# Performance work log

Hardware: AMD Instinct MI355X
Metric: run time of the kernel (lower is better)

Reference implementation:

```python
import jax, jax.numpy as jnp
import numpy as np

NUM_BINS = 128  # 32 mid-band bins + 96 bottom-band bins
LN_EPS = 1e-5


def _mlp_scores(desc, W1, b1, g1, be1, W2, b2, Ws, bs):
    # Linear -> LayerNorm -> SiLU -> Linear -> score head
    h = desc @ W1 + b1
    mu = h.mean(-1, keepdims=True)
    var = h.var(-1, keepdims=True)
    h = (h - mu) * jax.lax.rsqrt(var + LN_EPS) * g1 + be1
    h = h * jax.nn.sigmoid(h)  # SiLU
    feat = h @ W2 + b2
    scores = (feat @ Ws + bs)[..., 0]  # [B, N]
    return scores


def _grid_ids(kpts, H, W):
    x = kpts[..., 0]
    y = kpts[..., 1]
    mid = (y > 0.2 * H) & (y <= 0.5 * H)
    btm = y > 0.5 * H
    mgx = jnp.clip((x / W * 8).astype(jnp.int32), 0, 7)
    mgy = jnp.clip(((y - 0.2 * H) / (0.3 * H) * 4).astype(jnp.int32), 0, 3)
    bgx = jnp.clip((x / W * 16).astype(jnp.int32), 0, 15)
    bgy = jnp.clip(((y - 0.5 * H) / (0.5 * H) * 6).astype(jnp.int32), 0, 5)
    gid = jnp.where(btm, 32 + bgy * 16 + bgx, jnp.where(mid, mgy * 8 + mgx, -1))
    return gid  # [B, N], -1 = not in any grid band


def _select_one(scores, gid, top_k):
    # strict-'>' loop in the original), then compact + top-k fallback.
    N = scores.shape[0]
    valid = gid >= 0
    seg = jnp.where(valid, gid, NUM_BINS)  # dump invalid pts in dummy bin
    binmax = jax.ops.segment_max(scores, seg, num_segments=NUM_BINS + 1)
    is_win = valid & (scores == binmax[seg])
    winner_idx = jax.ops.segment_min(
        jnp.where(is_win, jnp.arange(N), N), seg, num_segments=NUM_BINS + 1
    )[:NUM_BINS]  # N = empty bin sentinel
    bin_valid = winner_idx < N
    # stable sort: non-empty bins first, preserving bin order
    order = jnp.argsort((~bin_valid).astype(jnp.int32))
    winners = winner_idx[order]  # [NUM_BINS], trailing sentinels
    num_sel = jnp.sum(bin_valid)
    # mask out already-selected winners, top-k fallback on the rest
    win_mask = jnp.zeros(N, bool).at[jnp.where(bin_valid, winner_idx, N)].set(True, mode='drop')
    rem = jnp.where(win_mask, -1e10, scores)
    _, extra = jax.lax.top_k(rem, top_k)
    j = jnp.arange(top_k)
    sel = jnp.where(
        j < num_sel,
        winners[jnp.clip(j, 0, NUM_BINS - 1)],
        extra[jnp.clip(j - num_sel, 0, top_k - 1)],
    )
    return sel  # [top_k]


def setup_inputs() -> dict:
    key = jax.random.key(0)
    ks = jax.random.split(key, 4)
    B, N, IN, OUT = 8, 50000, 256, 128
    H, W = 376, 1241
    kpts = jax.random.uniform(ks[0], (B, N, 2), jnp.float32) * jnp.array([W, H], jnp.float32)
    desc = jax.random.normal(ks[1], (B, N, IN), jnp.float32)
    kw = jax.random.split(ks[2], 3)
    W1 = 0.01 * jax.random.normal(kw[0], (IN, 256), jnp.float32)
    b1 = jnp.zeros((256,), jnp.float32)
    g1 = jnp.ones((256,), jnp.float32)
    be1 = jnp.zeros((256,), jnp.float32)
    W2 = 0.01 * jax.random.normal(kw[1], (256, OUT), jnp.float32)
    b2 = jnp.zeros((OUT,), jnp.float32)
    Ws = 0.001 * jax.random.normal(kw[2], (OUT, 1), jnp.float32)
    bs = jnp.zeros((1,), jnp.float32)
    return {"kpts": kpts, "desc": desc, "H": H, "W": W, "top_k": 128,
            "W1": W1, "b1": b1, "g1": g1, "be1": be1,
            "W2": W2, "b2": b2, "Ws": Ws, "bs": bs}


def reference(kpts, desc, H, W, top_k, W1, b1, g1, be1, W2, b2, Ws, bs):
    scores = _mlp_scores(desc, W1, b1, g1, be1, W2, b2, Ws, bs)  # [B,N]
    gid = _grid_ids(kpts, H, W)  # [B,N]
    indices = jax.vmap(lambda s, g: _select_one(s, g, top_k))(scores, gid)  # [B,top_k]
    final_feat = jnp.take_along_axis(desc, indices[:, :, None], axis=1)  # [B,top_k,256]
    final_kpts = jnp.take_along_axis(kpts, indices[:, :, None], axis=1)  # [B,top_k,2]
    return final_feat, final_kpts, indices
```

## Files before the change

kernel.cpp:

```cpp
#include <hip/hip_runtime.h>

#define THREADS 256

typedef short bf16x8 __attribute__((ext_vector_type(8)));
typedef float f32x4 __attribute__((ext_vector_type(4)));

__device__ __forceinline__ unsigned short f2bf(float x) {
    unsigned u = __float_as_uint(x);
    return (unsigned short)((u + 0x7FFFu + ((u >> 16) & 1u)) >> 16);
}
__device__ __forceinline__ float bf2f(unsigned short h) {
    return __uint_as_float(((unsigned)h) << 16);
}
__device__ __forceinline__ unsigned score_key(float s) {
    unsigned u = __float_as_uint(s);
    return (u & 0x80000000u) ? ~u : (u | 0x80000000u);
}

__device__ __forceinline__ void split8(const float* __restrict__ f, bf16x8& hv, bf16x8& lv) {
    union { unsigned w[4]; bf16x8 v; } H, L;
#pragma unroll
    for (int q = 0; q < 4; ++q) {
        const float x0 = f[2 * q], x1 = f[2 * q + 1];
        const unsigned b0 = __float_as_uint(x0), b1_ = __float_as_uint(x1);
        const unsigned u0 = b0 + 0x7FFFu + ((b0 >> 16) & 1u);
        const unsigned u1 = b1_ + 0x7FFFu + ((b1_ >> 16) & 1u);
        const float h0 = __uint_as_float(u0 & 0xFFFF0000u);
        const float h1 = __uint_as_float(u1 & 0xFFFF0000u);
        const unsigned l0 = f2bf(x0 - h0), l1 = f2bf(x1 - h1);
        H.w[q] = (u0 >> 16) | ((u1 >> 16) << 16);
        L.w[q] = l0 | (l1 << 16);
    }
    hv = H.v; lv = L.v;
}

__device__ __forceinline__ void async_cp16(const uint4* g, uint4* l) {
    __builtin_amdgcn_global_load_lds(
        (const __attribute__((address_space(1))) unsigned int*)g,
        (__attribute__((address_space(3))) unsigned int*)l, 16, 0, 0);
}

__global__ void prep_kernel(const float* __restrict__ W2, const float* __restrict__ b2,
                            const float* __restrict__ Ws, const float* __restrict__ bs,
                            float* __restrict__ v, int OUT) {
    int j = threadIdx.x;
    float acc = 0.f;
    for (int o = 0; o < OUT; ++o) acc += W2[j * OUT + o] * Ws[o];
    v[j] = acc;
    if (j == 0) {
        float c = bs[0];
        for (int o = 0; o < OUT; ++o) c += b2[o] * Ws[o];
        v[256] = c;
    }
}

__global__ void prep_w1frag(const float* __restrict__ W1, uint4* __restrict__ wfrag) {
    const int s = blockIdx.x * 256 + threadIdx.x;
    const int rem = s & 2047;
    const int kt = s >> 11;
    const int c = rem >> 6;
    const int lane = rem & 63;
    const int h = c >> 4;
    const int nt = c & 15;
    const int col = nt * 16 + (lane & 15);
    const int kb = kt * 32 + (lane >> 4) * 8;
    unsigned pk[4];
#pragma unroll
    for (int q = 0; q < 4; ++q) {
        float x0 = W1[(size_t)(kb + 2 * q) * 256 + col];
        float x1 = W1[(size_t)(kb + 2 * q + 1) * 256 + col];
        unsigned short a0, a1;
        if (h == 0) { a0 = f2bf(x0); a1 = f2bf(x1); }
        else {
            a0 = f2bf(x0 - bf2f(f2bf(x0)));
            a1 = f2bf(x1 - bf2f(f2bf(x1)));
        }
        pk[q] = (unsigned)a0 | ((unsigned)a1 << 16);
    }
    wfrag[s] = make_uint4(pk[0], pk[1], pk[2], pk[3]);
}

__global__ void init_bins(unsigned long long* __restrict__ bins, int n) {
    int i = blockIdx.x * blockDim.x + threadIdx.x;
    if (i < n) bins[i] = 0ULL;
}

__global__ __launch_bounds__(256, 2) void score_kernel(
    const float* __restrict__ desc, const float* __restrict__ kpts,
    const uint4* __restrict__ wfrag,
    const float* __restrict__ b1, const float* __restrict__ g1, const float* __restrict__ be1,
    const int* __restrict__ Hp, const int* __restrict__ Wp,
    const float* __restrict__ v,
    float* __restrict__ scores, unsigned long long* __restrict__ bins,
    int N, int total)
{
    __shared__ uint4 BS[2][32 * 64];
    __shared__ float b1L[256], g1L[256], beL[256], vL[256];

    const int t = threadIdx.x;
    const int lane = t & 63;
    const int w = t >> 6;
    const int l15 = lane & 15, q4 = lane >> 4;
    const int wrow0 = blockIdx.x * 128 + w * 32;

    b1L[t] = b1[t]; g1L[t] = g1[t]; beL[t] = be1[t]; vL[t] = v[t];

    {
        const uint4* bsrc = wfrag + (w * 8) * 64 + lane;
#pragma unroll
        for (int j = 0; j < 8; ++j)
            async_cp16(bsrc + j * 64, &BS[0][(w * 8 + j) * 64]);
    }

    const int rA0 = min(wrow0 + l15, total - 1);
    const int rA1 = min(wrow0 + 16 + l15, total - 1);
    const float* pa0 = desc + (size_t)rA0 * 256 + q4 * 8;
    const float* pa1 = desc + (size_t)rA1 * 256 + q4 * 8;
    float4 a00 = *(const float4*)pa0, a01 = *(const float4*)(pa0 + 4);
    float4 a10 = *(const float4*)pa1, a11 = *(const float4*)(pa1 + 4);

    __syncthreads();

    f32x4 acc[2][16];
#pragma unroll
    for (int n = 0; n < 16; ++n) {
        const float bc = b1L[n * 16 + l15];
        acc[0][n] = (f32x4){bc, bc, bc, bc};
        acc[1][n] = (f32x4){bc, bc, bc, bc};
    }

    for (int kt = 0; kt < 8; ++kt) {
        const int cur = kt & 1;
        if (kt < 7) {
            const uint4* bsrc = wfrag + (size_t)(kt + 1) * 2048 + (w * 8) * 64 + lane;
#pragma unroll
            for (int j = 0; j < 8; ++j)
                async_cp16(bsrc + j * 64, &BS[cur ^ 1][(w * 8 + j) * 64]);
        }
        bf16x8 ah[2], al[2];
        {
            float f0[8] = {a00.x, a00.y, a00.z, a00.w, a01.x, a01.y, a01.z, a01.w};
            split8(f0, ah[0], al[0]);
            float f1[8] = {a10.x, a10.y, a10.z, a10.w, a11.x, a11.y, a11.z, a11.w};
            split8(f1, ah[1], al[1]);
        }
        if (kt < 7) {
            const float* q0 = pa0 + (kt + 1) * 32;
            const float* q1 = pa1 + (kt + 1) * 32;
            a00 = *(const float4*)q0; a01 = *(const float4*)(q0 + 4);
            a10 = *(const float4*)q1; a11 = *(const float4*)(q1 + 4);
        }
#pragma unroll
        for (int g = 0; g < 4; ++g) {
            bf16x8 bh[4], bl[4];
#pragma unroll
            for (int j = 0; j < 4; ++j) {
                bh[j] = *(const bf16x8*)&BS[cur][(g * 4 + j) * 64 + lane];
                bl[j] = *(const bf16x8*)&BS[cur][(16 + g * 4 + j) * 64 + lane];
            }
#pragma unroll
            for (int p = 0; p < 4; ++p) {
#pragma unroll
                for (int j = 0; j < 4; ++j)
#pragma unroll
                    for (int m = 0; m < 2; ++m) {
                        const bf16x8 aa = (p & 2) ? al[m] : ah[m];
                        const bf16x8 bb = (p & 1) ? bl[j] : bh[j];
                        acc[m][g * 4 + j] =
                            __builtin_amdgcn_mfma_f32_16x16x32_bf16(aa, bb, acc[m][g * 4 + j], 0, 0, 0);
                    }
            }
        }
        __syncthreads();
    }

    const float Wf = (float)Wp[0];
    const int Hi = Hp[0];
    const float t02 = (float)(0.2 * (double)Hi);
    const float t05 = (float)(0.5 * (double)Hi);
    const float t03 = (float)(0.3 * (double)Hi);
    const float cterm = v[256];

#pragma unroll
    for (int m = 0; m < 2; ++m)
#pragma unroll
        for (int r = 0; r < 4; ++r) {
            float sx = 0.f, sq = 0.f;
#pragma unroll
            for (int n = 0; n < 16; ++n) {
                const float x = acc[m][n][r];
                sx += x; sq = fmaf(x, x, sq);
            }
#pragma unroll
            for (int mask = 1; mask <= 8; mask <<= 1) {
                sx += __shfl_xor(sx, mask);
                sq += __shfl_xor(sq, mask);
            }
            const float mu = sx * (1.f / 256.f);
            const float var = sq * (1.f / 256.f) - mu * mu;
            const float rs = 1.f / sqrtf(var + 1e-5f);
            float dot = 0.f;
#pragma unroll
            for (int n = 0; n < 16; ++n) {
                const int c = n * 16 + l15;
                const float hv = (acc[m][n][r] - mu) * rs * g1L[c] + beL[c];
                const float sg = 1.f / (1.f + __expf(-hv));
                dot = fmaf(vL[c], hv * sg, dot);
            }
#pragma unroll
            for (int mask = 1; mask <= 8; mask <<= 1) dot += __shfl_xor(dot, mask);

            if (l15 == 0) {
                const int row = wrow0 + m * 16 + q4 * 4 + r;
                if (row < total) {
                    const float sc = dot + cterm;
                    scores[row] = sc;
                    const float x = kpts[(size_t)row * 2 + 0];
                    const float y = kpts[(size_t)row * 2 + 1];
                    int g = -1;
                    if (y > t05) {
                        int bgx = (int)(x / Wf * 16.f); bgx = min(max(bgx, 0), 15);
                        int bgy = (int)((y - t05) / t05 * 6.f); bgy = min(max(bgy, 0), 5);
                        g = 32 + bgy * 16 + bgx;
                    } else if (y > t02) {
                        int mgx = (int)(x / Wf * 8.f); mgx = min(max(mgx, 0), 7);
                        int mgy = (int)((y - t02) / t03 * 4.f); mgy = min(max(mgy, 0), 3);
                        g = mgy * 8 + mgx;
                    }
                    if (g >= 0) {
                        const int bb = row / N;
                        const int n = row - bb * N;
                        const unsigned long long pk =
                            ((unsigned long long)score_key(sc) << 32) | (unsigned)(~(unsigned)n);
                        atomicMax(&bins[bb * 128 + g], pk);
                    }
                }
            }
        }
}

__global__ __launch_bounds__(256) void finalize_kernel(
    const float* __restrict__ scores, const unsigned long long* __restrict__ bins,
    const float* __restrict__ desc, const float* __restrict__ kpts,
    const int* __restrict__ tkp, float* __restrict__ out, int B, int N)
{
    const int b = blockIdx.x, t = threadIdx.x;
    const int topk = tkp[0];
    __shared__ int selL[512];
    __shared__ int nselS;
    __shared__ unsigned long long red[256];
    __shared__ unsigned long long binL[128];

    if (t < 128) binL[t] = bins[b * 128 + t];
    __syncthreads();
    if (t == 0) {
        int c = 0;
        for (int i = 0; i < 128; ++i)
            if ((binL[i] >> 32) != 0ULL) selL[c++] = (int)(~(unsigned)binL[i]);
        nselS = c;
    }
    __syncthreads();
    const int nsel = nselS;

    for (int need = nsel; need < topk; ++need) {
        unsigned long long best = 0ULL;
        for (int i = t; i < N; i += THREADS) {
            bool taken = false;
            for (int s2 = 0; s2 < need; ++s2)
                if (selL[s2] == i) { taken = true; break; }
            if (!taken) {
                const unsigned long long pk =
                    ((unsigned long long)score_key(scores[(size_t)b * N + i]) << 32)
                    | (unsigned)(~(unsigned)i);
                if (pk > best) best = pk;
            }
        }
        red[t] = best;
        __syncthreads();
        for (int off = 128; off > 0; off >>= 1) {
            if (t < off) { if (red[t + off] > red[t]) red[t] = red[t + off]; }
            __syncthreads();
        }
        if (t == 0) selL[need] = (int)(~(unsigned)red[0]);
        __syncthreads();
    }

    float* o_feat = out;
    float* o_kpts = out + (size_t)B * topk * 256;
    float* o_idx  = out + (size_t)B * topk * 258;
    for (int e = t; e < topk * 64; e += THREADS) {
        const int j = e >> 6, q4 = e & 63;
        const int n = selL[j];
        *(float4*)&o_feat[((size_t)b * topk + j) * 256 + q4 * 4] =
            *(const float4*)&desc[((size_t)b * N + n) * 256 + q4 * 4];
    }
    for (int j = t; j < topk; j += THREADS) {
        const int n = selL[j];
        o_kpts[((size_t)b * topk + j) * 2 + 0] = kpts[((size_t)b * N + n) * 2 + 0];
        o_kpts[((size_t)b * topk + j) * 2 + 1] = kpts[((size_t)b * N + n) * 2 + 1];
        o_idx[(size_t)b * topk + j] = (float)n;
    }
}

extern "C" void kernel_launch(void* const* d_in, const int* in_sizes, int n_in,
                              void* d_out, int out_size, void* d_ws, size_t ws_size,
                              hipStream_t stream) {
    const float* kpts = (const float*)d_in[0];
    const float* desc = (const float*)d_in[1];
    const int*   Hp   = (const int*)d_in[2];
    const int*   Wp   = (const int*)d_in[3];
    const int*   tkp  = (const int*)d_in[4];
    const float* W1   = (const float*)d_in[5];
    const float* b1   = (const float*)d_in[6];
    const float* g1   = (const float*)d_in[7];
    const float* be1  = (const float*)d_in[8];
    const float* W2   = (const float*)d_in[9];
    const float* b2   = (const float*)d_in[10];
    const float* Ws   = (const float*)d_in[11];
    const float* bs   = (const float*)d_in[12];

    const int total = in_sizes[1] / 256;
    const int BT    = out_size / 259;
    const int B     = BT / 128;
    const int N     = total / B;
    const int OUT   = in_sizes[11];

    float* ws_v      = (float*)d_ws;
    float* ws_scores = ws_v + 512;
    size_t off = ((size_t)(512 + total) * 4 + 255) & ~(size_t)255;
    unsigned long long* ws_bins = (unsigned long long*)((char*)d_ws + off);
    size_t off2 = (off + (size_t)B * 128 * 8 + 255) & ~(size_t)255;
    uint4* ws_wfrag = (uint4*)((char*)d_ws + off2);

    prep_kernel<<<1, 256, 0, stream>>>(W2, b2, Ws, bs, ws_v, OUT);
    prep_w1frag<<<64, 256, 0, stream>>>(W1, ws_wfrag);
    init_bins<<<(B * 128 + 255) / 256, 256, 0, stream>>>(ws_bins, B * 128);
    score_kernel<<<(total + 127) / 128, 256, 0, stream>>>(
        desc, kpts, ws_wfrag, b1, g1, be1, Hp, Wp, ws_v, ws_scores, ws_bins, N, total);
    finalize_kernel<<<B, 256, 0, stream>>>(ws_scores, ws_bins, desc, kpts, tkp,
                                           (float*)d_out, B, N);
}
```

Before: 430.4 us.

## Switch score GEMM to 32x32x16 MFMA with re-laid-out W1 fragments

Each wave's 32-row tile now uses 32x32x16 bf16 MFMA instructions instead of two 16-row tiles of 16x16x32. The W1 fragment layout in the prep kernel is rebuilt to match, and the LayerNorm/SiLU epilogue is rewritten for the 32x32 accumulator layout with wider shuffle reductions. It also uses the library bf16 conversion for the hi/lo split and raises wave priority around the MFMA bursts. The aim is to cut LDS reads of B fragments and per-instruction overhead in the split-precision GEMM, at the cost of more accumulator registers per lane and a more complex row mapping.

```diff
diff --git a/kernel.cpp b/kernel.cpp
--- a/kernel.cpp
+++ b/kernel.cpp
@@ -1,9 +1,10 @@
 #include <hip/hip_runtime.h>
+#include <hip/hip_bf16.h>
 
 #define THREADS 256
 
 typedef short bf16x8 __attribute__((ext_vector_type(8)));
-typedef float f32x4 __attribute__((ext_vector_type(4)));
+typedef float f32x16 __attribute__((ext_vector_type(16)));
 
 __device__ __forceinline__ unsigned short f2bf(float x) {
     unsigned u = __float_as_uint(x);
@@ -17,19 +18,18 @@
     return (u & 0x80000000u) ? ~u : (u | 0x80000000u);
 }
 
-__device__ __forceinline__ void split8(const float* __restrict__ f, bf16x8& hv, bf16x8& lv) {
-    union { unsigned w[4]; bf16x8 v; } H, L;
-#pragma unroll
-    for (int q = 0; q < 4; ++q) {
-        const float x0 = f[2 * q], x1 = f[2 * q + 1];
-        const unsigned b0 = __float_as_uint(x0), b1_ = __float_as_uint(x1);
-        const unsigned u0 = b0 + 0x7FFFu + ((b0 >> 16) & 1u);
-        const unsigned u1 = b1_ + 0x7FFFu + ((b1_ >> 16) & 1u);
-        const float h0 = __uint_as_float(u0 & 0xFFFF0000u);
-        const float h1 = __uint_as_float(u1 & 0xFFFF0000u);
-        const unsigned l0 = f2bf(x0 - h0), l1 = f2bf(x1 - h1);
-        H.w[q] = (u0 >> 16) | ((u1 >> 16) << 16);
-        L.w[q] = l0 | (l1 << 16);
+__device__ __forceinline__ void split8n(const float4& fa, const float4& fb,
+                                        bf16x8& hv, bf16x8& lv) {
+    const float f[8] = {fa.x, fa.y, fa.z, fa.w, fb.x, fb.y, fb.z, fb.w};
+    union { unsigned short u[8]; bf16x8 v; } H, L;
+#pragma unroll
+    for (int j = 0; j < 8; ++j) {
+        __hip_bfloat16 hb = __float2bfloat16(f[j]);
+        const unsigned short hr = reinterpret_cast<const unsigned short&>(hb);
+        const float hf = __uint_as_float(((unsigned)hr) << 16);
+        __hip_bfloat16 lb = __float2bfloat16(f[j] - hf);
+        H.u[j] = hr;
+        L.u[j] = reinterpret_cast<const unsigned short&>(lb);
     }
     hv = H.v; lv = L.v;
 }
@@ -56,21 +56,21 @@
 
 __global__ void prep_w1frag(const float* __restrict__ W1, uint4* __restrict__ wfrag) {
     const int s = blockIdx.x * 256 + threadIdx.x;
-    const int rem = s & 2047;
     const int kt = s >> 11;
-    const int c = rem >> 6;
-    const int lane = rem & 63;
-    const int h = c >> 4;
-    const int nt = c & 15;
-    const int col = nt * 16 + (lane & 15);
-    const int kb = kt * 32 + (lane >> 4) * 8;
+    const int c = (s >> 6) & 31;
+    const int lane = s & 63;
+    const int hl = c >> 4;
+    const int nt = (c >> 1) & 7;
+    const int kc = c & 1;
+    const int col = nt * 32 + (lane & 31);
+    const int k0 = kt * 32 + kc * 16 + (lane >> 5) * 8;
     unsigned pk[4];
 #pragma unroll
     for (int q = 0; q < 4; ++q) {
-        float x0 = W1[(size_t)(kb + 2 * q) * 256 + col];
-        float x1 = W1[(size_t)(kb + 2 * q + 1) * 256 + col];
+        float x0 = W1[(size_t)(k0 + 2 * q) * 256 + col];
+        float x1 = W1[(size_t)(k0 + 2 * q + 1) * 256 + col];
         unsigned short a0, a1;
-        if (h == 0) { a0 = f2bf(x0); a1 = f2bf(x1); }
+        if (hl == 0) { a0 = f2bf(x0); a1 = f2bf(x1); }
         else {
             a0 = f2bf(x0 - bf2f(f2bf(x0)));
             a1 = f2bf(x1 - bf2f(f2bf(x1)));
@@ -100,7 +100,8 @@
     const int t = threadIdx.x;
     const int lane = t & 63;
     const int w = t >> 6;
-    const int l15 = lane & 15, q4 = lane >> 4;
+    const int c31 = lane & 31;
+    const int h = lane >> 5;
     const int wrow0 = blockIdx.x * 128 + w * 32;
 
     b1L[t] = b1[t]; g1L[t] = g1[t]; beL[t] = be1[t]; vL[t] = v[t];
@@ -112,21 +113,21 @@
             async_cp16(bsrc + j * 64, &BS[0][(w * 8 + j) * 64]);
     }
 
-    const int rA0 = min(wrow0 + l15, total - 1);
-    const int rA1 = min(wrow0 + 16 + l15, total - 1);
-    const float* pa0 = desc + (size_t)rA0 * 256 + q4 * 8;
-    const float* pa1 = desc + (size_t)rA1 * 256 + q4 * 8;
-    float4 a00 = *(const float4*)pa0, a01 = *(const float4*)(pa0 + 4);
-    float4 a10 = *(const float4*)pa1, a11 = *(const float4*)(pa1 + 4);
+    const int rA = min(wrow0 + c31, total - 1);
+    const float* pa = desc + (size_t)rA * 256 + h * 8;
+    float4 aA = *(const float4*)(pa + 0);
+    float4 aB = *(const float4*)(pa + 4);
+    float4 aC = *(const float4*)(pa + 16);
+    float4 aD = *(const float4*)(pa + 20);
 
     __syncthreads();
 
-    f32x4 acc[2][16];
-#pragma unroll
-    for (int n = 0; n < 16; ++n) {
-        const float bc = b1L[n * 16 + l15];
-        acc[0][n] = (f32x4){bc, bc, bc, bc};
-        acc[1][n] = (f32x4){bc, bc, bc, bc};
+    f32x16 acc[8];
+#pragma unroll
+    for (int nt = 0; nt < 8; ++nt) {
+        const float bc = b1L[nt * 32 + c31];
+#pragma unroll
+        for (int r = 0; r < 16; ++r) acc[nt][r] = bc;
     }
 
     for (int kt = 0; kt < 8; ++kt) {
@@ -137,40 +138,67 @@
             for (int j = 0; j < 8; ++j)
                 async_cp16(bsrc + j * 64, &BS[cur ^ 1][(w * 8 + j) * 64]);
         }
-        bf16x8 ah[2], al[2];
+        float4 nA, nB, nC, nD;
+        if (kt < 7) {
+            const float* q = pa + (kt + 1) * 32;
+            nA = *(const float4*)(q + 0);  nB = *(const float4*)(q + 4);
+            nC = *(const float4*)(q + 16); nD = *(const float4*)(q + 20);
+        }
         {
-            float f0[8] = {a00.x, a00.y, a00.z, a00.w, a01.x, a01.y, a01.z, a01.w};
-            split8(f0, ah[0], al[0]);
-            float f1[8] = {a10.x, a10.y, a10.z, a10.w, a11.x, a11.y, a11.z, a11.w};
-            split8(f1, ah[1], al[1]);
-        }
-        if (kt < 7) {
-            const float* q0 = pa0 + (kt + 1) * 32;
-            const float* q1 = pa1 + (kt + 1) * 32;
-            a00 = *(const float4*)q0; a01 = *(const float4*)(q0 + 4);
-            a10 = *(const float4*)q1; a11 = *(const float4*)(q1 + 4);
-        }
-#pragma unroll
-        for (int g = 0; g < 4; ++g) {
-            bf16x8 bh[4], bl[4];
-#pragma unroll
-            for (int j = 0; j < 4; ++j) {
-                bh[j] = *(const bf16x8*)&BS[cur][(g * 4 + j) * 64 + lane];
-                bl[j] = *(const bf16x8*)&BS[cur][(16 + g * 4 + j) * 64 + lane];
-            }
-#pragma unroll
-            for (int p = 0; p < 4; ++p) {
-#pragma unroll
-                for (int j = 0; j < 4; ++j)
-#pragma unroll
-                    for (int m = 0; m < 2; ++m) {
-                        const bf16x8 aa = (p & 2) ? al[m] : ah[m];
-                        const bf16x8 bb = (p & 1) ? bl[j] : bh[j];
-                        acc[m][g * 4 + j] =
-                            __builtin_amdgcn_mfma_f32_16x16x32_bf16(aa, bb, acc[m][g * 4 + j], 0, 0, 0);
-                    }
-            }
-        }
+            bf16x8 ah, al;
+            split8n(aA, aB, ah, al);
+            bf16x8 bq[8];
+#pragma unroll
+            for (int nt = 0; nt < 8; ++nt)
+                bq[nt] = *(const bf16x8*)&BS[cur][(nt * 2 + 0) * 64 + lane];
+            __builtin_amdgcn_s_setprio(1);
+#pragma unroll
+            for (int nt = 0; nt < 8; ++nt)
+                acc[nt] = __builtin_amdgcn_mfma_f32_32x32x16_bf16(ah, bq[nt], acc[nt], 0, 0, 0);
+#pragma unroll
+            for (int nt = 0; nt < 8; ++nt)
+                acc[nt] = __builtin_amdgcn_mfma_f32_32x32x16_bf16(al, bq[nt], acc[nt], 0, 0, 0);
+            __builtin_amdgcn_s_setprio(0);
+#pragma unroll
+            for (int nt = 0; nt < 8; ++nt)
+                bq[nt] = *(const bf16x8*)&BS[cur][(16 + nt * 2 + 0) * 64 + lane];
+            __builtin_amdgcn_s_setprio(1);
+#pragma unroll
+            for (int nt = 0; nt < 8; ++nt)
+                acc[nt] = __builtin_amdgcn_mfma_f32_32x32x16_bf16(ah, bq[nt], acc[nt], 0, 0, 0);
+#pragma unroll
+            for (int nt = 0; nt < 8; ++nt)
+                acc[nt] = __builtin_amdgcn_mfma_f32_32x32x16_bf16(al, bq[nt], acc[nt], 0, 0, 0);
+            __builtin_amdgcn_s_setprio(0);
+        }
+        {
+            bf16x8 ah, al;
+            split8n(aC, aD, ah, al);
+            bf16x8 bq[8];
+#pragma unroll
+            for (int nt = 0; nt < 8; ++nt)
+                bq[nt] = *(const bf16x8*)&BS[cur][(nt * 2 + 1) * 64 + lane];
+            __builtin_amdgcn_s_setprio(1);
+#pragma unroll
+            for (int nt = 0; nt < 8; ++nt)
+                acc[nt] = __builtin_amdgcn_mfma_f32_32x32x16_bf16(ah, bq[nt], acc[nt], 0, 0, 0);
+#pragma unroll
+            for (int nt = 0; nt < 8; ++nt)
+                acc[nt] = __builtin_amdgcn_mfma_f32_32x32x16_bf16(al, bq[nt], acc[nt], 0, 0, 0);
+            __builtin_amdgcn_s_setprio(0);
+#pragma unroll
+            for (int nt = 0; nt < 8; ++nt)
+                bq[nt] = *(const bf16x8*)&BS[cur][(16 + nt * 2 + 1) * 64 + lane];
+            __builtin_amdgcn_s_setprio(1);
+#pragma unroll
+            for (int nt = 0; nt < 8; ++nt)
+                acc[nt] = __builtin_amdgcn_mfma_f32_32x32x16_bf16(ah, bq[nt], acc[nt], 0, 0, 0);
+#pragma unroll
+            for (int nt = 0; nt < 8; ++nt)
+                acc[nt] = __builtin_amdgcn_mfma_f32_32x32x16_bf16(al, bq[nt], acc[nt], 0, 0, 0);
+            __builtin_amdgcn_s_setprio(0);
+        }
+        aA = nA; aB = nB; aC = nC; aD = nD;
         __syncthreads();
     }
 
@@ -182,61 +210,59 @@
     const float cterm = v[256];
 
 #pragma unroll
-    for (int m = 0; m < 2; ++m)
-#pragma unroll
-        for (int r = 0; r < 4; ++r) {
-            float sx = 0.f, sq = 0.f;
-#pragma unroll
-            for (int n = 0; n < 16; ++n) {
-                const float x = acc[m][n][r];
-                sx += x; sq = fmaf(x, x, sq);
-            }
-#pragma unroll
-            for (int mask = 1; mask <= 8; mask <<= 1) {
-                sx += __shfl_xor(sx, mask);
-                sq += __shfl_xor(sq, mask);
-            }
-            const float mu = sx * (1.f / 256.f);
-            const float var = sq * (1.f / 256.f) - mu * mu;
-            const float rs = 1.f / sqrtf(var + 1e-5f);
-            float dot = 0.f;
-#pragma unroll
-            for (int n = 0; n < 16; ++n) {
-                const int c = n * 16 + l15;
-                const float hv = (acc[m][n][r] - mu) * rs * g1L[c] + beL[c];
-                const float sg = 1.f / (1.f + __expf(-hv));
-                dot = fmaf(vL[c], hv * sg, dot);
-            }
-#pragma unroll
-            for (int mask = 1; mask <= 8; mask <<= 1) dot += __shfl_xor(dot, mask);
-
-            if (l15 == 0) {
-                const int row = wrow0 + m * 16 + q4 * 4 + r;
-                if (row < total) {
-                    const float sc = dot + cterm;
-                    scores[row] = sc;
-                    const float x = kpts[(size_t)row * 2 + 0];
-                    const float y = kpts[(size_t)row * 2 + 1];
-                    int g = -1;
-                    if (y > t05) {
-                        int bgx = (int)(x / Wf * 16.f); bgx = min(max(bgx, 0), 15);
-                        int bgy = (int)((y - t05) / t05 * 6.f); bgy = min(max(bgy, 0), 5);
-                        g = 32 + bgy * 16 + bgx;
-                    } else if (y > t02) {
-                        int mgx = (int)(x / Wf * 8.f); mgx = min(max(mgx, 0), 7);
-                        int mgy = (int)((y - t02) / t03 * 4.f); mgy = min(max(mgy, 0), 3);
-                        g = mgy * 8 + mgx;
-                    }
-                    if (g >= 0) {
-                        const int bb = row / N;
-                        const int n = row - bb * N;
-                        const unsigned long long pk =
-                            ((unsigned long long)score_key(sc) << 32) | (unsigned)(~(unsigned)n);
-                        atomicMax(&bins[bb * 128 + g], pk);
-                    }
+    for (int reg = 0; reg < 16; ++reg) {
+        float sx = 0.f, sq = 0.f;
+#pragma unroll
+        for (int nt = 0; nt < 8; ++nt) {
+            const float x = acc[nt][reg];
+            sx += x; sq = fmaf(x, x, sq);
+        }
+#pragma unroll
+        for (int m = 1; m <= 16; m <<= 1) {
+            sx += __shfl_xor(sx, m);
+            sq += __shfl_xor(sq, m);
+        }
+        const float mu = sx * (1.f / 256.f);
+        const float var = sq * (1.f / 256.f) - mu * mu;
+        const float rs = 1.f / sqrtf(var + 1e-5f);
+        float dot = 0.f;
+#pragma unroll
+        for (int nt = 0; nt < 8; ++nt) {
+            const int c = nt * 32 + c31;
+            const float hv = (acc[nt][reg] - mu) * rs * g1L[c] + beL[c];
+            const float sg = 1.f / (1.f + __expf(-hv));
+            dot = fmaf(vL[c], hv * sg, dot);
+        }
+#pragma unroll
+        for (int m = 1; m <= 16; m <<= 1) dot += __shfl_xor(dot, m);
+
+        if (c31 == 0) {
+            const int row = wrow0 + (reg & 3) + 8 * (reg >> 2) + 4 * h;
+            if (row < total) {
+                const float sc = dot + cterm;
+                scores[row] = sc;
+                const float x = kpts[(size_t)row * 2 + 0];
+                const float y = kpts[(size_t)row * 2 + 1];
+                int g = -1;
+                if (y > t05) {
+                    int bgx = (int)(x / Wf * 16.f); bgx = min(max(bgx, 0), 15);
+                    int bgy = (int)((y - t05) / t05 * 6.f); bgy = min(max(bgy, 0), 5);
+                    g = 32 + bgy * 16 + bgx;
+                } else if (y > t02) {
+                    int mgx = (int)(x / Wf * 8.f); mgx = min(max(mgx, 0), 7);
+                    int mgy = (int)((y - t02) / t03 * 4.f); mgy = min(max(mgy, 0), 3);
+                    g = mgy * 8 + mgx;
+                }
+                if (g >= 0) {
+                    const int bb = row / N;
+                    const int n = row - bb * N;
+                    const unsigned long long pk =
+                        ((unsigned long long)score_key(sc) << 32) | (unsigned)(~(unsigned)n);
+                    atomicMax(&bins[bb * 128 + g], pk);
                 }
             }
         }
+    }
 }
 
 __global__ __launch_bounds__(256) void finalize_kernel(
```

Result: slower. 501.1 us (+16.4%).
